# Optimization experiments

Hardware: AMD Instinct MI355X
Metric: run time of the kernel (lower is better)

## Reference

```python
import jax, jax.numpy as jnp
import numpy as np

N, E = 100000, 800000
D_IN, D_HID, D_OUT = 128, 128, 40


def _lin_params(key, d_out, d_in, bias):
    k1, k2 = jax.random.split(key)
    bound = 1.0 / np.sqrt(d_in)
    W = jax.random.uniform(k1, (d_out, d_in), jnp.float32, -bound, bound)
    if bias:
        b = jax.random.uniform(k2, (d_out,), jnp.float32, -bound, bound)
        return W, b
    return W


def setup_inputs() -> dict:
    key = jax.random.key(0)
    ks = jax.random.split(key, 8)
    x = jax.random.normal(ks[0], (N, D_IN), jnp.float32)
    edge_index = jax.random.randint(ks[1], (2, E), 0, N, jnp.int64)
    Wl0, b0 = _lin_params(ks[2], D_HID, D_IN, True)
    Wr0 = _lin_params(ks[3], D_HID, D_IN, False)
    Wl1, b1 = _lin_params(ks[4], D_HID, D_HID, True)
    Wr1 = _lin_params(ks[5], D_HID, D_HID, False)
    Wl2, b2 = _lin_params(ks[6], D_OUT, D_HID, True)
    Wr2 = _lin_params(ks[7], D_OUT, D_HID, False)
    return {"x": x, "edge_index": edge_index,
            "Wl0": Wl0, "Wr0": Wr0, "b0": b0,
            "Wl1": Wl1, "Wr1": Wr1, "b1": b1,
            "Wl2": Wl2, "Wr2": Wr2, "b2": b2}


def _sage_conv(x, src, dst, Wl, Wr, b):
    # mean aggregation of neighbor messages (src -> dst), PyG SAGEConv semantics
    msg = x[src]                                               # [E, d]
    agg = jax.ops.segment_sum(msg, dst, num_segments=N)        # [N, d]
    deg = jax.ops.segment_sum(jnp.ones((src.shape[0],), x.dtype), dst,
                              num_segments=N)                  # [N]
    agg = agg / jnp.maximum(deg, 1.0)[:, None]
    # out = lin_l(agg) + lin_r(x); lin_l has bias, lin_r does not
    return agg @ Wl.T + x @ Wr.T + b


def reference(x, edge_index, Wl0, Wr0, b0, Wl1, Wr1, b1, Wl2, Wr2, b2):
    src, dst = edge_index[0], edge_index[1]
    h = jax.nn.relu(_sage_conv(x, src, dst, Wl0, Wr0, b0))   # dropout = identity in eval
    h = jax.nn.relu(_sage_conv(h, src, dst, Wl1, Wr1, b1))
    h = _sage_conv(h, src, dst, Wl2, Wr2, b2)
    return jax.nn.log_softmax(h, axis=1)
```

## Files before the change

kernel.cpp:

```cpp
#include <hip/hip_runtime.h>
#include <hip/hip_bf16.h>
#include <math.h>

#define D 128
typedef unsigned int uint;
typedef unsigned short ushort;

using bf16x8 = __attribute__((ext_vector_type(8))) short;
using f32x4  = __attribute__((ext_vector_type(4))) float;
using f32x2  = __attribute__((ext_vector_type(2))) float;

static __device__ __forceinline__ ushort f2b(float f) {
    __hip_bfloat16 h = __float2bfloat16(f);
    return __builtin_bit_cast(ushort, h);
}
static __device__ __forceinline__ float blo(uint u) {
    uint v = u << 16;
    return __builtin_bit_cast(float, v);
}
static __device__ __forceinline__ float bhi(uint u) {
    uint v = u & 0xFFFF0000u;
    return __builtin_bit_cast(float, v);
}

__global__ __launch_bounds__(256) void k_prep(
    const int* __restrict__ dst, int* __restrict__ deg, int* __restrict__ pos, int E,
    const float* __restrict__ x, ushort* __restrict__ Abuf, int n4,
    const float* __restrict__ Wl0, const float* __restrict__ Wr0,
    const float* __restrict__ Wl1, const float* __restrict__ Wr1,
    const float* __restrict__ Wl2, const float* __restrict__ Wr2,
    ushort* __restrict__ Wtg0, ushort* __restrict__ Wtg1,
    ushort* __restrict__ W2tg)
{
    int i = blockIdx.x * 256 + threadIdx.x;
    int p = -1;
    if (i < E) p = atomicAdd(&deg[dst[i]], 1);
    if (i < n4) {
        float4 v = *(const float4*)(x + (size_t)i * 4);
        int node = i >> 5;
        int coff = (i & 31) * 4;
        ushort4 o;
        o.x = f2b(v.x); o.y = f2b(v.y); o.z = f2b(v.z); o.w = f2b(v.w);
        *(ushort4*)(Abuf + (size_t)node * 256 + 128 + coff) = o;
    }
    if (i < 2 * 128 * 256) {
        int which = i >> 15;
        int o = i & 32767;
        int j = o >> 8, k = o & 255;
        const float* Wl = which ? Wl1 : Wl0;
        const float* Wr = which ? Wr1 : Wr0;
        float v = (k < 128) ? Wl[j * 128 + k] : Wr[j * 128 + (k - 128)];
        (which ? Wtg1 : Wtg0)[o] = f2b(v);
    } else if (i < 2 * 128 * 256 + 80 * 128) {
        int o = i - 2 * 128 * 256;
        int j = o >> 7, k = o & 127;
        float v = (j < 40) ? Wl2[j * 128 + k] : Wr2[(j - 40) * 128 + k];
        W2tg[o] = f2b(v);
    }
    if (i < E) pos[i] = p;
}

__global__ void k_scan1(const int* __restrict__ deg, int* __restrict__ rowptr,
                        int* __restrict__ bsum, int nN) {
    __shared__ int s[256];
    int tid = threadIdx.x;
    int i = blockIdx.x * 256 + tid;
    int v = (i < nN) ? deg[i] : 0;
    s[tid] = v;
    __syncthreads();
#pragma unroll
    for (int o = 1; o < 256; o <<= 1) {
        int t = (tid >= o) ? s[tid - o] : 0;
        __syncthreads();
        s[tid] += t;
        __syncthreads();
    }
    if (i < nN) rowptr[i] = s[tid] - v;
    if (tid == 255) bsum[blockIdx.x] = s[255];
}

__global__ void k_scan2(int* __restrict__ bsum, int nb) {
    __shared__ int s[512];
    __shared__ int carry_s;
    int tid = threadIdx.x;
    if (tid == 0) carry_s = 0;
    __syncthreads();
    for (int base = 0; base < nb; base += 512) {
        int i = base + tid;
        int v = (i < nb) ? bsum[i] : 0;
        s[tid] = v;
        __syncthreads();
#pragma unroll
        for (int o = 1; o < 512; o <<= 1) {
            int t = (tid >= o) ? s[tid - o] : 0;
            __syncthreads();
            s[tid] += t;
            __syncthreads();
        }
        int carry = carry_s;
        if (i < nb) bsum[i] = s[tid] - v + carry;
        int total = s[511];
        __syncthreads();
        if (tid == 0) carry_s = carry + total;
        __syncthreads();
    }
}

__global__ void k_scan3(int* __restrict__ rowptr, const int* __restrict__ bsum,
                        int nN, int E) {
    int i = blockIdx.x * 256 + threadIdx.x;
    if (i < nN) rowptr[i] = rowptr[i] + bsum[blockIdx.x];
    if (i == 0) rowptr[nN] = E;
}

__global__ void k_place2(const int* __restrict__ src, const int* __restrict__ dst,
                         const int* __restrict__ rowptr, const int* __restrict__ pos,
                         int* __restrict__ col, int E) {
    int e = blockIdx.x * 256 + threadIdx.x;
    if (e < E) col[rowptr[dst[e]] + pos[e]] = src[e];
}

__global__ __launch_bounds__(256) void k_gather128(
    const ushort* __restrict__ feat, ushort* __restrict__ agg,
    const int* __restrict__ rowptr, const int* __restrict__ col, int nN)
{
    int tid = threadIdx.x;
    int lane = tid & 63;
    int h = lane >> 5;
    int node = blockIdx.x * 8 + ((tid >> 6) << 1) + h;
    if (node >= nN) return;
    int g = (lane >> 4) & 1;
    int r = lane & 15;
    int beg = rowptr[node], end = rowptr[node + 1];
    const char* fb = (const char*)feat;
    const uint rb = (uint)(r << 4);
    float a[8];
#pragma unroll
    for (int i = 0; i < 8; ++i) a[i] = 0.f;

    int j = beg + g;
    for (; j + 2 < end; j += 4) {
        int s0 = col[j], s1 = col[j + 2];
        uint4 v0 = *(const uint4*)(fb + (((uint)s0 << 9) + rb));
        uint4 v1 = *(const uint4*)(fb + (((uint)s1 << 9) + rb));
        const uint* p0 = (const uint*)&v0;
        const uint* p1 = (const uint*)&v1;
#pragma unroll
        for (int i = 0; i < 4; ++i) {
            a[2 * i]     += blo(p0[i]) + blo(p1[i]);
            a[2 * i + 1] += bhi(p0[i]) + bhi(p1[i]);
        }
    }
    if (j < end) {
        int s0 = col[j];
        uint4 v0 = *(const uint4*)(fb + (((uint)s0 << 9) + rb));
        const uint* p0 = (const uint*)&v0;
#pragma unroll
        for (int i = 0; i < 4; ++i) {
            a[2 * i]     += blo(p0[i]);
            a[2 * i + 1] += bhi(p0[i]);
        }
    }
#pragma unroll
    for (int i = 0; i < 8; ++i)
        a[i] += __shfl_xor(a[i], 16);
    if (g == 0) {
        float inv = 1.0f / (float)max(end - beg, 1);
        uint4 o;
        uint* po = (uint*)&o;
#pragma unroll
        for (int i = 0; i < 4; ++i)
            po[i] = (uint)f2b(a[2 * i] * inv) | ((uint)f2b(a[2 * i + 1] * inv) << 16);
        *(uint4*)(agg + (size_t)node * 256 + r * 8) = o;
    }
}

template<int OUTJ, int KDIM, int SW, int MODE>
__global__ __launch_bounds__(256) void k_gemm_mfma(
    const ushort* __restrict__ A, int astride,
    const ushort* __restrict__ Wt, const float* __restrict__ bias,
    ushort* __restrict__ out, int ostride, ushort* __restrict__ out2, int nN)
{
    constexpr int NT = OUTJ / 16;
    constexpr int KSTEPS = KDIM / 32;
    __shared__ __align__(16) ushort Ws[OUTJ * SW];

    const int tid = threadIdx.x;
    constexpr int CHUNKS = OUTJ * KDIM / 8;
#pragma unroll
    for (int c = tid; c < CHUNKS; c += 256) {
        int row = c / (KDIM / 8);
        int ko  = (c % (KDIM / 8)) * 8;
        *(uint4*)(Ws + row * SW + ko) = *(const uint4*)(Wt + row * KDIM + ko);
    }
    __syncthreads();

    const int l = tid & 63, wv = tid >> 6;
    const int q = l >> 4, r = l & 15;
    const long long m0 = (long long)blockIdx.x * 128 + wv * 32;
    const int mA = (int)min(m0 + r, (long long)(nN - 1));
    const int mB = (int)min(m0 + 16 + r, (long long)(nN - 1));
    const ushort* pa = A + (size_t)mA * astride + q * 8;
    const ushort* pb = A + (size_t)mB * astride + q * 8;

    f32x4 acc[2][NT];
#pragma unroll
    for (int mt = 0; mt < 2; ++mt)
#pragma unroll
        for (int nt = 0; nt < NT; ++nt)
            acc[mt][nt] = (f32x4){0.f, 0.f, 0.f, 0.f};

    bf16x8 a0 = *(const bf16x8*)pa;
    bf16x8 a1 = *(const bf16x8*)pb;
#pragma unroll
    for (int ks = 0; ks < KSTEPS; ++ks) {
        bf16x8 a0n = a0, a1n = a1;
        if (ks + 1 < KSTEPS) {
            a0n = *(const bf16x8*)(pa + (ks + 1) * 32);
            a1n = *(const bf16x8*)(pb + (ks + 1) * 32);
        }
#pragma unroll
        for (int nt = 0; nt < NT; ++nt) {
            bf16x8 b = *(const bf16x8*)(Ws + (nt * 16 + r) * SW + ks * 32 + q * 8);
            acc[0][nt] = __builtin_amdgcn_mfma_f32_16x16x32_bf16(a0, b, acc[0][nt], 0, 0, 0);
            acc[1][nt] = __builtin_amdgcn_mfma_f32_16x16x32_bf16(a1, b, acc[1][nt], 0, 0, 0);
        }
        a0 = a0n; a1 = a1n;
    }

#pragma unroll
    for (int mt = 0; mt < 2; ++mt) {
#pragma unroll
        for (int i = 0; i < 4; ++i) {
            long long m = m0 + mt * 16 + q * 4 + i;
            if (m >= nN) continue;
#pragma unroll
            for (int nt = 0; nt < NT; ++nt) {
                int cc = nt * 16 + r;
                float v = acc[mt][nt][i];
                if (MODE == 0) {
                    v += bias[cc];
                    v = fmaxf(v, 0.f);
                    out[(size_t)m * ostride + cc] = f2b(v);
                } else {
                    if (cc < 40) out[(size_t)m * 40 + cc] = f2b(v);
                    else { v += bias[cc - 40]; out2[(size_t)m * 40 + (cc - 40)] = f2b(v); }
                }
            }
        }
    }
}

__global__ __launch_bounds__(256) void k_gather40_lsm(
    const ushort* __restrict__ P, const ushort* __restrict__ R,
    const int* __restrict__ rowptr, const int* __restrict__ col,
    float* __restrict__ out, int nN)
{
    int tid = threadIdx.x;
    int lane = tid & 63;
    int h = lane >> 4;
    int node = blockIdx.x * 16 + ((tid >> 6) << 2) + h;
    if (node >= nN) return;
    int g = (lane >> 3) & 1;
    int r = lane & 7;
    int beg = rowptr[node], end = rowptr[node + 1];
    const char* pbase = (const char*)P;
    const uint rb = (uint)(r << 4);
    f32x2 a2[4];
#pragma unroll
    for (int i = 0; i < 4; ++i) a2[i] = (f32x2){0.f, 0.f};

    int j = beg + g;
    for (; j + 2 < end; j += 4) {
        int s0 = col[j], s1 = col[j + 2];
        uint4 v0 = *(const uint4*)(pbase + ((((uint)s0 * 5u) << 4) + rb));
        uint4 v1 = *(const uint4*)(pbase + ((((uint)s1 * 5u) << 4) + rb));
        const uint* p0 = (const uint*)&v0;
        const uint* p1 = (const uint*)&v1;
#pragma unroll
        for (int i = 0; i < 4; ++i)
            a2[i] += (f32x2){blo(p0[i]) + blo(p1[i]), bhi(p0[i]) + bhi(p1[i])};
    }
    if (j < end) {
        int s0 = col[j];
        uint4 v0 = *(const uint4*)(pbase + ((((uint)s0 * 5u) << 4) + rb));
        const uint* p0 = (const uint*)&v0;
#pragma unroll
        for (int i = 0; i < 4; ++i)
            a2[i] += (f32x2){blo(p0[i]), bhi(p0[i])};
    }
    float a[8];
#pragma unroll
    for (int i = 0; i < 4; ++i) { a[2 * i] = a2[i].x; a[2 * i + 1] = a2[i].y; }
#pragma unroll
    for (int i = 0; i < 8; ++i)
        a[i] += __shfl_xor(a[i], 8);
    float inv = 1.0f / (float)max(end - beg, 1);
    uint4 rv = *(const uint4*)(R + (size_t)node * 40 + r * 8);
    const uint* pr = (const uint*)&rv;
    float vv[8];
    float mx = -INFINITY;
#pragma unroll
    for (int i = 0; i < 8; ++i) {
        float rc = (i & 1) ? bhi(pr[i >> 1]) : blo(pr[i >> 1]);
        int c = r * 8 + i;
        vv[i] = (c < 40) ? (a[i] * inv + rc) : -INFINITY;
        mx = fmaxf(mx, vv[i]);
    }
    mx = fmaxf(mx, __shfl_xor(mx, 1));
    mx = fmaxf(mx, __shfl_xor(mx, 2));
    mx = fmaxf(mx, __shfl_xor(mx, 4));
    float s = 0.f;
#pragma unroll
    for (int i = 0; i < 8; ++i) {
        int c = r * 8 + i;
        if (c < 40) s += __expf(vv[i] - mx);
    }
    s += __shfl_xor(s, 1);
    s += __shfl_xor(s, 2);
    s += __shfl_xor(s, 4);
    float lse = mx + __logf(s);
    if (g == 0 && r < 5) {
        float4 o0 = make_float4(vv[0] - lse, vv[1] - lse, vv[2] - lse, vv[3] - lse);
        float4 o1 = make_float4(vv[4] - lse, vv[5] - lse, vv[6] - lse, vv[7] - lse);
        *(float4*)(out + (size_t)node * 40 + r * 8)     = o0;
        *(float4*)(out + (size_t)node * 40 + r * 8 + 4) = o1;
    }
}

extern "C" void kernel_launch(void* const* d_in, const int* in_sizes, int n_in,
                              void* d_out, int out_size, void* d_ws, size_t ws_size,
                              hipStream_t stream) {
    const float* x   = (const float*)d_in[0];
    const int*   ei  = (const int*)d_in[1];
    const float* Wl0 = (const float*)d_in[2];
    const float* Wr0 = (const float*)d_in[3];
    const float* b0  = (const float*)d_in[4];
    const float* Wl1 = (const float*)d_in[5];
    const float* Wr1 = (const float*)d_in[6];
    const float* b1  = (const float*)d_in[7];
    const float* Wl2 = (const float*)d_in[8];
    const float* Wr2 = (const float*)d_in[9];
    const float* b2  = (const float*)d_in[10];
    const int nN = in_sizes[0] / D;
    const int E  = in_sizes[1] / 2;
    const int* src = ei;
    const int* dst = ei + E;

    char* w = (char*)d_ws;
    auto alloc = [&](size_t bytes) { char* p = w; w += (bytes + 255) & ~(size_t)255; return p; };
    int*    deg    = (int*)   alloc((size_t)nN * 4);
    int*    rowptr = (int*)   alloc((size_t)(nN + 1) * 4);
    int*    bsum   = (int*)   alloc((size_t)((nN + 255) / 256) * 4);
    int*    col    = (int*)   alloc((size_t)E * 4);
    ushort* AbufA  = (ushort*)alloc((size_t)nN * 256 * 2);
    ushort* AbufB  = (ushort*)alloc((size_t)nN * 256 * 2);
    ushort* Wtg0   = (ushort*)alloc((size_t)128 * 256 * 2);
    ushort* Wtg1   = (ushort*)alloc((size_t)128 * 256 * 2);
    ushort* W2tg   = (ushort*)alloc((size_t)80 * 128 * 2);
    int*    pos    = (int*)AbufB;
    ushort* Pbuf   = AbufB;
    ushort* Rbuf   = AbufB + (size_t)nN * 40;
    float*  logits = (float*)d_out;

    const int NB        = (nN + 255) / 256;
    const int GATH_BLKS = (nN + 7) / 8;
    const int G40_BLKS  = (nN + 15) / 16;
    const int GEMM_BLKS = (nN + 127) / 128;
    const int n4        = nN * 32;
    int prep_max = n4;
    if (E > prep_max) prep_max = E;
    const int PREP_BLKS = (prep_max + 255) / 256;

    hipMemsetAsync(deg, 0, (size_t)nN * 4, stream);
    k_prep  <<<PREP_BLKS, 256, 0, stream>>>(dst, deg, pos, E, x, AbufA, n4,
                                            Wl0, Wr0, Wl1, Wr1, Wl2, Wr2,
                                            Wtg0, Wtg1, W2tg);
    k_scan1 <<<NB, 256, 0, stream>>>(deg, rowptr, bsum, nN);
    k_scan2 <<<1, 512, 0, stream>>>(bsum, NB);
    k_scan3 <<<NB, 256, 0, stream>>>(rowptr, bsum, nN, E);
    k_place2<<<(E + 255) / 256, 256, 0, stream>>>(src, dst, rowptr, pos, col, E);

    k_gather128<<<GATH_BLKS, 256, 0, stream>>>(AbufA + 128, AbufA, rowptr, col, nN);
    k_gemm_mfma<128, 256, 264, 0><<<GEMM_BLKS, 256, 0, stream>>>(
        AbufA, 256, Wtg0, b0, AbufB + 128, 256, nullptr, nN);

    k_gather128<<<GATH_BLKS, 256, 0, stream>>>(AbufB + 128, AbufB, rowptr, col, nN);
    k_gemm_mfma<128, 256, 264, 0><<<GEMM_BLKS, 256, 0, stream>>>(
        AbufB, 256, Wtg1, b1, AbufA + 128, 256, nullptr, nN);

    k_gemm_mfma<80, 128, 136, 1><<<GEMM_BLKS, 256, 0, stream>>>(
        AbufA + 128, 256, W2tg, b2, Pbuf, 40, Rbuf, nN);
    k_gather40_lsm<<<G40_BLKS, 256, 0, stream>>>(Pbuf, Rbuf, rowptr, col, logits, nN);
}
```

Measured before the change: 321.6 us.

## Build CSR via two-level bucket sort instead of global atomics and scans

Replaces the CSR construction (global atomic degree count, three-kernel scan, scatter placement) with a two-level bucketed counting sort. Edges are first histogrammed into coarse buckets of 1024 nodes per block in shared memory, scanned, and placed into an intermediate edge buffer. A per-bucket kernel then does a fine shared-memory histogram, scan and placement into col. This targets contended global atomics and random global scatters, but adds a single-block scan, an extra pass over the edges, and a limit of 128 buckets (nN up to about 131k).

```diff
diff --git a/kernel.cpp b/kernel.cpp
--- a/kernel.cpp
+++ b/kernel.cpp
@@ -23,8 +23,12 @@
     return __builtin_bit_cast(float, v);
 }
 
-__global__ __launch_bounds__(256) void k_prep(
-    const int* __restrict__ dst, int* __restrict__ deg, int* __restrict__ pos, int E,
+#define NBLK_A 1024
+#define MAXB   128
+#define WTOT   (2*128*256 + 80*128)
+
+__global__ __launch_bounds__(256) void k_bcount(
+    const int* __restrict__ dst, int* __restrict__ cnt, int E, int nbuck,
     const float* __restrict__ x, ushort* __restrict__ Abuf, int n4,
     const float* __restrict__ Wl0, const float* __restrict__ Wr0,
     const float* __restrict__ Wl1, const float* __restrict__ Wr1,
@@ -32,92 +36,118 @@
     ushort* __restrict__ Wtg0, ushort* __restrict__ Wtg1,
     ushort* __restrict__ W2tg)
 {
-    int i = blockIdx.x * 256 + threadIdx.x;
-    int p = -1;
-    if (i < E) p = atomicAdd(&deg[dst[i]], 1);
-    if (i < n4) {
+    __shared__ int h[MAXB];
+    int tid = threadIdx.x, b = blockIdx.x;
+    for (int k = tid; k < nbuck; k += 256) h[k] = 0;
+    __syncthreads();
+    int chunk = (E + NBLK_A - 1) / NBLK_A;
+    int beg = b * chunk, end = min(beg + chunk, E);
+    for (int e = beg + tid; e < end; e += 256)
+        atomicAdd(&h[dst[e] >> 10], 1);
+    __syncthreads();
+    for (int k = tid; k < nbuck; k += 256) cnt[k * NBLK_A + b] = h[k];
+
+    for (int i = b * 256 + tid; i < n4; i += NBLK_A * 256) {
         float4 v = *(const float4*)(x + (size_t)i * 4);
-        int node = i >> 5;
-        int coff = (i & 31) * 4;
+        int node = i >> 5, coff = (i & 31) * 4;
         ushort4 o;
         o.x = f2b(v.x); o.y = f2b(v.y); o.z = f2b(v.z); o.w = f2b(v.w);
         *(ushort4*)(Abuf + (size_t)node * 256 + 128 + coff) = o;
     }
-    if (i < 2 * 128 * 256) {
-        int which = i >> 15;
-        int o = i & 32767;
-        int j = o >> 8, k = o & 255;
-        const float* Wl = which ? Wl1 : Wl0;
-        const float* Wr = which ? Wr1 : Wr0;
-        float v = (k < 128) ? Wl[j * 128 + k] : Wr[j * 128 + (k - 128)];
-        (which ? Wtg1 : Wtg0)[o] = f2b(v);
-    } else if (i < 2 * 128 * 256 + 80 * 128) {
-        int o = i - 2 * 128 * 256;
-        int j = o >> 7, k = o & 127;
-        float v = (j < 40) ? Wl2[j * 128 + k] : Wr2[(j - 40) * 128 + k];
-        W2tg[o] = f2b(v);
-    }
-    if (i < E) pos[i] = p;
-}
-
-__global__ void k_scan1(const int* __restrict__ deg, int* __restrict__ rowptr,
-                        int* __restrict__ bsum, int nN) {
-    __shared__ int s[256];
+    for (int i = b * 256 + tid; i < WTOT; i += NBLK_A * 256) {
+        if (i < 2 * 128 * 256) {
+            int which = i >> 15;
+            int o = i & 32767;
+            int j = o >> 8, kk = o & 255;
+            const float* Wl = which ? Wl1 : Wl0;
+            const float* Wr = which ? Wr1 : Wr0;
+            float v = (kk < 128) ? Wl[j * 128 + kk] : Wr[j * 128 + (kk - 128)];
+            (which ? Wtg1 : Wtg0)[o] = f2b(v);
+        } else {
+            int o = i - 2 * 128 * 256;
+            int j = o >> 7, kk = o & 127;
+            float v = (j < 40) ? Wl2[j * 128 + kk] : Wr2[(j - 40) * 128 + kk];
+            W2tg[o] = f2b(v);
+        }
+    }
+}
+
+__global__ __launch_bounds__(1024) void k_bscan(int* __restrict__ cnt,
+                                                int* __restrict__ bb,
+                                                int n, int nbuck, int E) {
+    __shared__ int s[1024];
     int tid = threadIdx.x;
-    int i = blockIdx.x * 256 + tid;
-    int v = (i < nN) ? deg[i] : 0;
-    s[tid] = v;
-    __syncthreads();
-#pragma unroll
-    for (int o = 1; o < 256; o <<= 1) {
+    int per = (n + 1023) >> 10;
+    int beg = tid * per, end = min(beg + per, n);
+    int sum = 0;
+    for (int i = beg; i < end; ++i) sum += cnt[i];
+    s[tid] = sum;
+    __syncthreads();
+#pragma unroll
+    for (int o = 1; o < 1024; o <<= 1) {
         int t = (tid >= o) ? s[tid - o] : 0;
         __syncthreads();
         s[tid] += t;
         __syncthreads();
     }
-    if (i < nN) rowptr[i] = s[tid] - v;
-    if (tid == 255) bsum[blockIdx.x] = s[255];
-}
-
-__global__ void k_scan2(int* __restrict__ bsum, int nb) {
-    __shared__ int s[512];
-    __shared__ int carry_s;
-    int tid = threadIdx.x;
-    if (tid == 0) carry_s = 0;
-    __syncthreads();
-    for (int base = 0; base < nb; base += 512) {
-        int i = base + tid;
-        int v = (i < nb) ? bsum[i] : 0;
-        s[tid] = v;
+    int run = s[tid] - sum;
+    for (int i = beg; i < end; ++i) { int v = cnt[i]; cnt[i] = run; run += v; }
+    __syncthreads();
+    for (int k = tid; k < nbuck; k += 1024) bb[k] = cnt[k * NBLK_A];
+    if (tid == 0) bb[nbuck] = E;
+}
+
+__global__ __launch_bounds__(256) void k_bplace(
+    const int* __restrict__ src, const int* __restrict__ dst,
+    const int* __restrict__ cnt, uint2* __restrict__ ebuf, int E, int nbuck)
+{
+    __shared__ int cur[MAXB];
+    int tid = threadIdx.x, b = blockIdx.x;
+    for (int k = tid; k < nbuck; k += 256) cur[k] = cnt[k * NBLK_A + b];
+    __syncthreads();
+    int chunk = (E + NBLK_A - 1) / NBLK_A;
+    int beg = b * chunk, end = min(beg + chunk, E);
+    for (int e = beg + tid; e < end; e += 256) {
+        int d = dst[e];
+        int r = atomicAdd(&cur[d >> 10], 1);
+        ebuf[r] = make_uint2((uint)src[e], (uint)d);
+    }
+}
+
+__global__ __launch_bounds__(1024) void k_bfine(
+    const uint2* __restrict__ ebuf, const int* __restrict__ bb,
+    int* __restrict__ rowptr, int* __restrict__ col, int nN, int nbuck, int E)
+{
+    __shared__ int cnt2[1024];
+    __shared__ int sc[1024];
+    int k = blockIdx.x, tid = threadIdx.x;
+    int e0 = bb[k], e1 = bb[k + 1];
+    cnt2[tid] = 0;
+    __syncthreads();
+    for (int e = e0 + tid; e < e1; e += 1024)
+        atomicAdd(&cnt2[ebuf[e].y & 1023], 1);
+    __syncthreads();
+    int v = cnt2[tid];
+    sc[tid] = v;
+    __syncthreads();
+#pragma unroll
+    for (int o = 1; o < 1024; o <<= 1) {
+        int t = (tid >= o) ? sc[tid - o] : 0;
         __syncthreads();
-#pragma unroll
-        for (int o = 1; o < 512; o <<= 1) {
-            int t = (tid >= o) ? s[tid - o] : 0;
-            __syncthreads();
-            s[tid] += t;
-            __syncthreads();
-        }
-        int carry = carry_s;
-        if (i < nb) bsum[i] = s[tid] - v + carry;
-        int total = s[511];
+        sc[tid] += t;
         __syncthreads();
-        if (tid == 0) carry_s = carry + total;
-        __syncthreads();
-    }
-}
-
-__global__ void k_scan3(int* __restrict__ rowptr, const int* __restrict__ bsum,
-                        int nN, int E) {
-    int i = blockIdx.x * 256 + threadIdx.x;
-    if (i < nN) rowptr[i] = rowptr[i] + bsum[blockIdx.x];
-    if (i == 0) rowptr[nN] = E;
-}
-
-__global__ void k_place2(const int* __restrict__ src, const int* __restrict__ dst,
-                         const int* __restrict__ rowptr, const int* __restrict__ pos,
-                         int* __restrict__ col, int E) {
-    int e = blockIdx.x * 256 + threadIdx.x;
-    if (e < E) col[rowptr[dst[e]] + pos[e]] = src[e];
+    }
+    int excl = sc[tid] - v;
+    int node = k * 1024 + tid;
+    if (node < nN) rowptr[node] = e0 + excl;
+    if (k == nbuck - 1 && tid == 0) rowptr[nN] = E;
+    cnt2[tid] = e0 + excl;
+    __syncthreads();
+    for (int e = e0 + tid; e < e1; e += 1024) {
+        uint2 sd = ebuf[e];
+        int r = atomicAdd(&cnt2[sd.y & 1023], 1);
+        col[r] = (int)sd.x;
+    }
 }
 
 __global__ __launch_bounds__(256) void k_gather128(
@@ -349,37 +379,32 @@
 
     char* w = (char*)d_ws;
     auto alloc = [&](size_t bytes) { char* p = w; w += (bytes + 255) & ~(size_t)255; return p; };
-    int*    deg    = (int*)   alloc((size_t)nN * 4);
+    const int nbuck = (nN + 1023) >> 10;
+    int*    cnt    = (int*)   alloc((size_t)nbuck * NBLK_A * 4);
+    int*    bb     = (int*)   alloc((size_t)(nbuck + 1) * 4);
     int*    rowptr = (int*)   alloc((size_t)(nN + 1) * 4);
-    int*    bsum   = (int*)   alloc((size_t)((nN + 255) / 256) * 4);
     int*    col    = (int*)   alloc((size_t)E * 4);
     ushort* AbufA  = (ushort*)alloc((size_t)nN * 256 * 2);
     ushort* AbufB  = (ushort*)alloc((size_t)nN * 256 * 2);
     ushort* Wtg0   = (ushort*)alloc((size_t)128 * 256 * 2);
     ushort* Wtg1   = (ushort*)alloc((size_t)128 * 256 * 2);
     ushort* W2tg   = (ushort*)alloc((size_t)80 * 128 * 2);
-    int*    pos    = (int*)AbufB;
+    uint2*  ebuf   = (uint2*)AbufB;
     ushort* Pbuf   = AbufB;
     ushort* Rbuf   = AbufB + (size_t)nN * 40;
     float*  logits = (float*)d_out;
 
-    const int NB        = (nN + 255) / 256;
     const int GATH_BLKS = (nN + 7) / 8;
     const int G40_BLKS  = (nN + 15) / 16;
     const int GEMM_BLKS = (nN + 127) / 128;
     const int n4        = nN * 32;
-    int prep_max = n4;
-    if (E > prep_max) prep_max = E;
-    const int PREP_BLKS = (prep_max + 255) / 256;
-
-    hipMemsetAsync(deg, 0, (size_t)nN * 4, stream);
-    k_prep  <<<PREP_BLKS, 256, 0, stream>>>(dst, deg, pos, E, x, AbufA, n4,
-                                            Wl0, Wr0, Wl1, Wr1, Wl2, Wr2,
-                                            Wtg0, Wtg1, W2tg);
-    k_scan1 <<<NB, 256, 0, stream>>>(deg, rowptr, bsum, nN);
-    k_scan2 <<<1, 512, 0, stream>>>(bsum, NB);
-    k_scan3 <<<NB, 256, 0, stream>>>(rowptr, bsum, nN, E);
-    k_place2<<<(E + 255) / 256, 256, 0, stream>>>(src, dst, rowptr, pos, col, E);
+
+    k_bcount<<<NBLK_A, 256, 0, stream>>>(dst, cnt, E, nbuck, x, AbufA, n4,
+                                         Wl0, Wr0, Wl1, Wr1, Wl2, Wr2,
+                                         Wtg0, Wtg1, W2tg);
+    k_bscan <<<1, 1024, 0, stream>>>(cnt, bb, nbuck * NBLK_A, nbuck, E);
+    k_bplace<<<NBLK_A, 256, 0, stream>>>(src, dst, cnt, ebuf, E, nbuck);
+    k_bfine <<<nbuck, 1024, 0, stream>>>(ebuf, bb, rowptr, col, nN, nbuck, E);
 
     k_gather128<<<GATH_BLKS, 256, 0, stream>>>(AbufA + 128, AbufA, rowptr, col, nN);
     k_gemm_mfma<128, 256, 264, 0><<<GEMM_BLKS, 256, 0, stream>>>(
```

Result: slower. 453.4 us (+41.0%).
